# Kernel tuning notes

Hardware: AMD Instinct MI355X
Metric: run time of the kernel (lower is better)

## Reference

```python
import jax, jax.numpy as jnp
import numpy as np

N_IDS = 512            # number of distinct vessel label ids (0 = background)
VOL = (256, 256, 256)  # D, H, W


def setup_inputs() -> dict:
    key = jax.random.key(0)
    k_lab, k_coin, k_a, k_b, k_hide = jax.random.split(key, 5)
    # integer label volume [D,H,W], ids in [0, N_IDS)
    vessel_labels = jax.random.randint(k_lab, VOL, 0, N_IDS, dtype=jnp.int32)

    # --- build id -> (intensity, class) LUTs, mirroring the torch per-label loop ---
    # coin flip per id: True -> dark class (1), intensity ~ U(0, 0.5)
    #                   False -> bright class (2), intensity ~ U(1.5, 2.1)
    coin = jax.random.bernoulli(k_coin, 0.5, (N_IDS,))
    int_a = jax.random.uniform(k_a, (N_IDS,), minval=0.0, maxval=0.5)
    int_b = jax.random.uniform(k_b, (N_IDS,), minval=1.5, maxval=2.1)
    # prune_labels: hide roughly half of the ids (hidden ids behave like background)
    hide = jax.random.bernoulli(k_hide, 0.5, (N_IDS,))
    ids = jnp.arange(N_IDS)
    keep = jnp.logical_and(jnp.logical_not(hide), ids != 0)
    intensity_lut = jnp.where(keep, jnp.where(coin, int_a, int_b), 1.0).astype(jnp.float32)
    class_lut = jnp.where(keep, jnp.where(coin, 1, 2), 0).astype(jnp.int32)
    return {"vessel_labels": vessel_labels,
            "intensity_lut": intensity_lut,
            "class_lut": class_lut}


def reference(vessel_labels, intensity_lut, class_lut):
    # three RandomFlipTransform passes ~ independent per-axis flips (fixed key)
    flips = jax.random.bernoulli(jax.random.key(1), 0.5, (3,))
    x = vessel_labels
    x = jnp.where(flips[0], jnp.flip(x, axis=0), x)
    x = jnp.where(flips[1], jnp.flip(x, axis=1), x)
    x = jnp.where(flips[2], jnp.flip(x, axis=2), x)

    # fused LUT gather replacing the per-id masked_fill loop
    scaling_tensor = intensity_lut[x][None]                      # [1,D,H,W]
    cls = class_lut[x]                                           # [D,H,W]
    onehot = jnp.moveaxis(jax.nn.one_hot(cls, 3, dtype=jnp.float32), -1, 0)  # [3,D,H,W]
    return scaling_tensor, onehot
```

## Files before the change

kernel.cpp:

```cpp
#include <hip/hip_runtime.h>


constexpr int VOXELS = 256 * 256 * 256;

typedef int   iv4 __attribute__((ext_vector_type(4)));
typedef float fv4 __attribute__((ext_vector_type(4)));

static inline unsigned rotl32(unsigned x, unsigned r) {
    return (x << r) | (x >> (32u - r));
}

static void threefry2x32(unsigned k0, unsigned k1, unsigned c0, unsigned c1,
                         unsigned* o0, unsigned* o1) {
    const unsigned rotA[4] = {13u, 15u, 26u, 6u};
    const unsigned rotB[4] = {17u, 29u, 16u, 24u};
    unsigned ks[3] = {k0, k1, k0 ^ k1 ^ 0x1BD11BDAu};
    unsigned x0 = c0 + ks[0];
    unsigned x1 = c1 + ks[1];
    for (int g = 0; g < 5; ++g) {
        const unsigned* rot = ((g & 1) == 0) ? rotA : rotB;
        for (int r = 0; r < 4; ++r) {
            x0 += x1;
            x1 = rotl32(x1, rot[r]);
            x1 ^= x0;
        }
        x0 += ks[(g + 1) % 3];
        x1 += ks[(g + 2) % 3] + (unsigned)(g + 1);
    }
    *o0 = x0;
    *o1 = x1;
}

static int jax_flip_bit(unsigned i) {
    unsigned o0, o1;
    threefry2x32(0u, 1u, 0u, i, &o0, &o1);
    return (((o0 ^ o1) >> 31) == 0u) ? 1 : 0;
}

__global__ __launch_bounds__(256) void VesselIntensitySynth_kernel(
    const int* __restrict__ labels,
    const float* __restrict__ ilut,
    const int* __restrict__ clut,
    float* __restrict__ out,
    const int f0, const int f1, const int f2)
{
    __shared__ unsigned lut[512];
    for (int i = threadIdx.x; i < 512; i += 256) {
        const unsigned ib = __float_as_uint(ilut[i]);
        lut[i] = (ib & ~3u) | (unsigned)clut[i];
    }
    __syncthreads();

    const int tid  = blockIdx.x * 256 + threadIdx.x;
    const int wid  = tid >> 6;
    const int lane = tid & 63;

    const int wbase = wid << 10;
    const int w  = lane << 2;
    const int h0 = (wbase >> 8) & 255;
    const int d  = wbase >> 16;

    const int sd = f0 ? (255 - d) : d;
    const int sw = f2 ? (252 - w) : w;
    const int sdw = (sd << 16) | sw;

    iv4 labs[4];
#pragma unroll
    for (int j = 0; j < 4; ++j) {
        const int sh = f1 ? (255 - (h0 + j)) : (h0 + j);
        labs[j] = *reinterpret_cast<const iv4*>(labels + (sdw | (sh << 8)));
    }

    unsigned pw[4][4];
#pragma unroll
    for (int j = 0; j < 4; ++j) {
        iv4 lab = labs[j];
        if (f2) {
            int tmp = lab.x; lab.x = lab.w; lab.w = tmp;
            tmp = lab.y;     lab.y = lab.z; lab.z = tmp;
        }
        pw[j][0] = lut[lab.x];
        pw[j][1] = lut[lab.y];
        pw[j][2] = lut[lab.z];
        pw[j][3] = lut[lab.w];
    }

    {
        float* p = out + wbase + w;
#pragma unroll
        for (int j = 0; j < 4; ++j) {
            fv4 s;
            s.x = __uint_as_float(pw[j][0] & ~3u);
            s.y = __uint_as_float(pw[j][1] & ~3u);
            s.z = __uint_as_float(pw[j][2] & ~3u);
            s.w = __uint_as_float(pw[j][3] & ~3u);
            *reinterpret_cast<fv4*>(p + (j << 8)) = s;
        }
    }
#pragma unroll
    for (int cls = 0; cls < 3; ++cls) {
        float* p = out + (cls + 1) * VOXELS + wbase + w;
#pragma unroll
        for (int j = 0; j < 4; ++j) {
            fv4 s;
            s.x = ((pw[j][0] & 3u) == (unsigned)cls) ? 1.0f : 0.0f;
            s.y = ((pw[j][1] & 3u) == (unsigned)cls) ? 1.0f : 0.0f;
            s.z = ((pw[j][2] & 3u) == (unsigned)cls) ? 1.0f : 0.0f;
            s.w = ((pw[j][3] & 3u) == (unsigned)cls) ? 1.0f : 0.0f;
            *reinterpret_cast<fv4*>(p + (j << 8)) = s;
        }
    }
}

extern "C" void kernel_launch(void* const* d_in, const int* in_sizes, int n_in,
                              void* d_out, int out_size, void* d_ws, size_t ws_size,
                              hipStream_t stream) {
    const int*   labels = (const int*)  d_in[0];
    const float* ilut   = (const float*)d_in[1];
    const int*   clut   = (const int*)  d_in[2];
    float*       out    = (float*)      d_out;

    const int f0 = jax_flip_bit(0u);
    const int f1 = jax_flip_bit(1u);
    const int f2 = jax_flip_bit(2u);

    const int threads = 256;
    const int blocks  = VOXELS / 16 / threads;
    VesselIntensitySynth_kernel<<<blocks, threads, 0, stream>>>(
        labels, ilut, clut, out, f0, f1, f2);
}
```

Before: 67.85 us.

## Split output planes across separate blocks instead of one block writing all four

Each block now handles one of the four output planes (intensity or one of three one-hot classes) for a 4096-voxel chunk, and four times as many blocks are launched. The intent is more parallelism and a single contiguous write stream per block. In exchange, each label chunk is read four times and the shared LUT is rebuilt four times as often. Adjacent blocks share the same slice, so cache reuse is relied on to absorb the redundant reads.

```diff
diff --git a/kernel.cpp b/kernel.cpp
--- a/kernel.cpp
+++ b/kernel.cpp
@@ -51,14 +51,15 @@
     }
     __syncthreads();
 
-    const int tid  = blockIdx.x * 256 + threadIdx.x;
-    const int wid  = tid >> 6;
-    const int lane = tid & 63;
+    const int plane    = blockIdx.x & 3;
+    const int sliceblk = blockIdx.x >> 2;
+    const int wave     = threadIdx.x >> 6;
+    const int lane     = threadIdx.x & 63;
 
-    const int wbase = wid << 10;
+    const int vbase = (sliceblk << 12) + (wave << 10);
     const int w  = lane << 2;
-    const int h0 = (wbase >> 8) & 255;
-    const int d  = wbase >> 16;
+    const int h0 = (vbase >> 8) & 255;
+    const int d  = vbase >> 16;
 
     const int sd = f0 ? (255 - d) : d;
     const int sw = f2 ? (252 - w) : w;
@@ -85,8 +86,8 @@
         pw[j][3] = lut[lab.w];
     }
 
-    {
-        float* p = out + wbase + w;
+    float* p = out + (size_t)plane * VOXELS + vbase + w;
+    if (plane == 0) {
 #pragma unroll
         for (int j = 0; j < 4; ++j) {
             fv4 s;
@@ -96,17 +97,15 @@
             s.w = __uint_as_float(pw[j][3] & ~3u);
             *reinterpret_cast<fv4*>(p + (j << 8)) = s;
         }
-    }
-#pragma unroll
-    for (int cls = 0; cls < 3; ++cls) {
-        float* p = out + (cls + 1) * VOXELS + wbase + w;
+    } else {
+        const unsigned cls = (unsigned)(plane - 1);
 #pragma unroll
         for (int j = 0; j < 4; ++j) {
             fv4 s;
-            s.x = ((pw[j][0] & 3u) == (unsigned)cls) ? 1.0f : 0.0f;
-            s.y = ((pw[j][1] & 3u) == (unsigned)cls) ? 1.0f : 0.0f;
-            s.z = ((pw[j][2] & 3u) == (unsigned)cls) ? 1.0f : 0.0f;
-            s.w = ((pw[j][3] & 3u) == (unsigned)cls) ? 1.0f : 0.0f;
+            s.x = ((pw[j][0] & 3u) == cls) ? 1.0f : 0.0f;
+            s.y = ((pw[j][1] & 3u) == cls) ? 1.0f : 0.0f;
+            s.z = ((pw[j][2] & 3u) == cls) ? 1.0f : 0.0f;
+            s.w = ((pw[j][3] & 3u) == cls) ? 1.0f : 0.0f;
             *reinterpret_cast<fv4*>(p + (j << 8)) = s;
         }
     }
@@ -125,7 +124,7 @@
     const int f2 = jax_flip_bit(2u);
 
     const int threads = 256;
-    const int blocks  = VOXELS / 16 / threads;
+    const int blocks  = 4 * (VOXELS / 16 / threads);
     VesselIntensitySynth_kernel<<<blocks, threads, 0, stream>>>(
         labels, ilut, clut, out, f0, f1, f2);
 }
```

New measurement: 79.48 us. +17.1%, slower.
